# Optimization experiments

Hardware: AMD Instinct MI355X
Metric: run time of the kernel (lower is better)

Reference implementation:

```python
import jax, jax.numpy as jnp
import numpy as np

INPUT_NDIMS = 1024
HIDDEN = 512
LATENT = 50
BATCH = 16384

def setup_inputs() -> dict:
    key = jax.random.key(0)
    ks = jax.random.split(key, 12)
    s = 0.02
    x = jax.random.uniform(ks[0], (BATCH, INPUT_NDIMS), dtype=jnp.float32)
    u = 0.01 + 0.98 * jax.random.uniform(ks[1], (BATCH, LATENT), dtype=jnp.float32)
    W1 = s * jax.random.normal(ks[2], (HIDDEN, INPUT_NDIMS), dtype=jnp.float32)
    b1 = jnp.zeros((HIDDEN,), jnp.float32)
    Wa = s * jax.random.normal(ks[3], (LATENT, HIDDEN), dtype=jnp.float32)
    ba = jnp.zeros((LATENT,), jnp.float32)
    Wb = s * jax.random.normal(ks[4], (LATENT, HIDDEN), dtype=jnp.float32)
    bb = jnp.zeros((LATENT,), jnp.float32)
    W2 = s * jax.random.normal(ks[5], (HIDDEN, LATENT), dtype=jnp.float32)
    b2 = jnp.zeros((HIDDEN,), jnp.float32)
    W3 = s * jax.random.normal(ks[6], (INPUT_NDIMS, HIDDEN), dtype=jnp.float32)
    b3 = jnp.zeros((INPUT_NDIMS,), jnp.float32)
    return dict(x=x, u=u, W1=W1, b1=b1, Wa=Wa, ba=ba, Wb=Wb, bb=bb, W2=W2, b2=b2, W3=W3, b3=b3)

def _stick_segments(v):
    # pi[:, k] = v[:, k] * prod_{j<k} (1 - v[:, j])  -- single O(K) cumprod pass
    cp = jnp.cumprod(1.0 - v, axis=1)                       # inclusive cumprod
    excl = jnp.concatenate([jnp.ones_like(cp[:, :1]), cp[:, :-1]], axis=1)
    return v * excl

def reference(x, u, W1, b1, Wa, ba, Wb, bb, W2, b2, W3, b3):
    # encoder: MLP -> positive Kumaraswamy params alpha (param1), beta (param2)
    h = jax.nn.relu(x @ W1.T + b1)                           # [B, H]
    alpha = jax.nn.softplus(h @ Wa.T + ba) + 1e-4            # [B, K]
    beta = jax.nn.softplus(h @ Wb.T + bb) + 1e-4             # [B, K]
    # Kumaraswamy reparameterized sample: v = (1 - u^(1/beta))^(1/alpha)
    v = jnp.power(1.0 - jnp.power(u, 1.0 / beta), 1.0 / alpha)
    # set_v_K_to_one: force last stick fraction to 1 so segments sum to 1
    v = v.at[:, -1].set(1.0)
    pi = _stick_segments(v)                                  # [B, K], rows sum to 1
    # decoder: MLP with sigmoid output
    h2 = jax.nn.relu(pi @ W2.T + b2)                         # [B, H]
    recon = jax.nn.sigmoid(h2 @ W3.T + b3)                   # [B, D]
    return recon, alpha, beta
```

## Files before the change

kernel.cpp:

```cpp
#include <hip/hip_runtime.h>
#include <hip/hip_bf16.h>

typedef __hip_bfloat16 bf16_t;
typedef __attribute__((ext_vector_type(4))) float f32x4;
typedef __attribute__((ext_vector_type(8))) __bf16 bf16x8;
typedef __attribute__((ext_vector_type(8))) short s16x8;
typedef __attribute__((ext_vector_type(4))) unsigned short u16x4;

#define BATCH 16384
#define NDIM  1024
#define HID   512
#define LAT   50

#define LOG2E 1.44269504088896340736f
#define RLOG2E 0.69314718055994530942f

__device__ __forceinline__ float ex2(float x) { return __builtin_amdgcn_exp2f(x); }
__device__ __forceinline__ float lg2(float x) { return __builtin_amdgcn_logf(x); }
__device__ __forceinline__ float rcp(float x) { return __builtin_amdgcn_rcpf(x); }

__device__ inline unsigned short f2b_u(float f) {
  union { bf16_t b; unsigned short u; } cv; cv.b = __float2bfloat16(f); return cv.u;
}

__device__ __forceinline__ void gload16(const void* src, void* dst_lds) {
  __builtin_amdgcn_global_load_lds(
      reinterpret_cast<const __attribute__((address_space(1))) void*>(
          reinterpret_cast<unsigned long long>(src)),
      reinterpret_cast<__attribute__((address_space(3))) void*>(
          static_cast<unsigned>(reinterpret_cast<unsigned long long>(dst_lds))),
      16, 0, 0);
}

#define WAIT_VMCNT(N)                                          \
  do {                                                         \
    asm volatile("s_waitcnt vmcnt(%0)" ::"i"(N) : "memory");   \
    __builtin_amdgcn_sched_barrier(0);                         \
  } while (0)

__global__ void prep_kernel(const float* __restrict__ x,  const float* __restrict__ W1,
                            const float* __restrict__ W3, const float* __restrict__ Wa,
                            const float* __restrict__ Wb, const float* __restrict__ W2,
                            const float* __restrict__ ba, const float* __restrict__ bb,
                            bf16_t* __restrict__ xb,  bf16_t* __restrict__ w1,
                            bf16_t* __restrict__ w3,  bf16_t* __restrict__ wab,
                            bf16_t* __restrict__ w2p, float* __restrict__ bab)
{
  const int XU   = (BATCH * NDIM) / 4;
  const int W1U  = (HID * NDIM) / 4;
  const int W3U  = (NDIM * HID) / 4;
  const int WABN = 128 * HID;
  const int W2PN = HID * 64;
  const int TOT  = XU + W1U + W3U + WABN + W2PN + 128;
  for (int i = blockIdx.x * blockDim.x + threadIdx.x; i < TOT;
       i += gridDim.x * blockDim.x) {
    int j = i;
    if (j < XU) {
      const f32x4 v = ((const f32x4*)x)[j];
      u16x4 o; o[0]=f2b_u(v[0]); o[1]=f2b_u(v[1]); o[2]=f2b_u(v[2]); o[3]=f2b_u(v[3]);
      ((u16x4*)xb)[j] = o; continue;
    }
    j -= XU;
    if (j < W1U) {
      const f32x4 v = ((const f32x4*)W1)[j];
      u16x4 o; o[0]=f2b_u(v[0]); o[1]=f2b_u(v[1]); o[2]=f2b_u(v[2]); o[3]=f2b_u(v[3]);
      ((u16x4*)w1)[j] = o; continue;
    }
    j -= W1U;
    if (j < W3U) {
      const f32x4 v = ((const f32x4*)W3)[j];
      u16x4 o; o[0]=f2b_u(v[0]); o[1]=f2b_u(v[1]); o[2]=f2b_u(v[2]); o[3]=f2b_u(v[3]);
      ((u16x4*)w3)[j] = o; continue;
    }
    j -= W3U;
    if (j < WABN) {
      const int n = j >> 9, k = j & 511;
      float v = (n < 50) ? Wa[n * 512 + k] : ((n < 100) ? Wb[(n - 50) * 512 + k] : 0.f);
      wab[j] = __float2bfloat16(v); continue;
    }
    j -= WABN;
    if (j < W2PN) {
      const int n = j >> 6, k = j & 63;
      w2p[j] = __float2bfloat16(k < 50 ? W2[n * 50 + k] : 0.f); continue;
    }
    j -= W2PN;
    bab[j] = (j < 50) ? ba[j] : ((j < 100) ? bb[j - 50] : 0.f);
  }
}

template<int EPI, int MT, int NT>
__global__ __launch_bounds__(512, 4)
void gemm_kernel(const bf16_t* __restrict__ A, const bf16_t* __restrict__ B,
                 const float* __restrict__ bias, void* __restrict__ out0,
                 int M, int N, int K)
{
  constexpr int MI  = MT / 32;
  constexpr int NI  = NT / 64;
  constexpr int IA  = MT / 64;
  constexpr int IB  = NT / 64;
  constexpr int L   = IA + IB;
  constexpr int BUF = MT * 128 + NT * 128;
  __shared__ char lds[2 * BUF];

  const int tid  = threadIdx.x;
  const int swzid = ((blockIdx.x & 7) * (gridDim.x >> 3)) + (blockIdx.x >> 3);
  const int nblocks = N / NT;
  const int bn   = swzid % nblocks;
  const int bm   = swzid / nblocks;
  const int wid  = tid >> 6;
  const int lane = tid & 63;
  const int l15  = lane & 15;
  const int l4   = lane >> 4;
  const int wm   = (wid >> 2) * (MT / 2);
  const int wn   = (wid & 3) * (NT / 4);
  const int uw   = __builtin_amdgcn_readfirstlane(wid);

  f32x4 acc[MI][NI] = {};

  auto stage = [&](char* buf, int k0) {
    #pragma unroll
    for (int i = 0; i < IA; ++i) {
      const int c  = (i * 8 + uw) * 64 + lane;
      const int r  = c >> 3;
      const int sp = c & 7;
      const int sl = sp ^ (r & 7);
      gload16(A + (size_t)(bm * MT + r) * K + k0 + sl * 8,
              buf + (i * 8 + uw) * 1024);
    }
    char* lB = buf + MT * 128;
    #pragma unroll
    for (int i = 0; i < IB; ++i) {
      const int c  = (i * 8 + uw) * 64 + lane;
      const int r  = c >> 3;
      const int sp = c & 7;
      const int sl = sp ^ (r & 7);
      gload16(B + (size_t)(bn * NT + r) * K + k0 + sl * 8,
              lB + (i * 8 + uw) * 1024);
    }
  };
  auto compute = [&](const char* buf) {
    const char* lA = buf;
    const char* lB = buf + MT * 128;
    #pragma unroll
    for (int h = 0; h < 2; ++h) {
      bf16x8 af[MI], bfr[NI];
      #pragma unroll
      for (int mi = 0; mi < MI; ++mi) {
        const int row = wm + mi * 16 + l15;
        const int sp  = (h * 4 + l4) ^ (row & 7);
        af[mi] = *(const bf16x8*)(lA + row * 128 + sp * 16);
      }
      #pragma unroll
      for (int ni = 0; ni < NI; ++ni) {
        const int row = wn + ni * 16 + l15;
        const int sp  = (h * 4 + l4) ^ (row & 7);
        bfr[ni] = *(const bf16x8*)(lB + row * 128 + sp * 16);
      }
      #pragma unroll
      for (int mi = 0; mi < MI; ++mi)
        #pragma unroll
        for (int ni = 0; ni < NI; ++ni)
          acc[mi][ni] = __builtin_amdgcn_mfma_f32_16x16x32_bf16(
              af[mi], bfr[ni], acc[mi][ni], 0, 0, 0);
    }
  };

  const int nt = K >> 6;
  stage(lds, 0);
  if (nt > 1) stage(lds + BUF, 64);
  for (int t = 0; t < nt; ++t) {
    if (t + 1 < nt) WAIT_VMCNT(L);
    else            WAIT_VMCNT(0);
    __builtin_amdgcn_s_barrier();
    compute(lds + (t & 1) * BUF);
    __builtin_amdgcn_s_barrier();
    __builtin_amdgcn_sched_barrier(0);
    if (t + 2 < nt) stage(lds + (t & 1) * BUF, (t + 2) << 6);
  }

  #pragma unroll
  for (int ni = 0; ni < NI; ++ni) {
    const int n  = bn * NT + wn + ni * 16 + l15;
    const float bv = bias[n];
    #pragma unroll
    for (int mi = 0; mi < MI; ++mi) {
      #pragma unroll
      for (int r = 0; r < 4; ++r) {
        const int m  = bm * MT + wm + mi * 16 + l4 * 4 + r;
        const float t = acc[mi][ni][r] + bv;
        if (EPI == 0) {
          ((bf16_t*)out0)[(size_t)m * N + n] = __float2bfloat16(fmaxf(t, 0.f));
        } else {
          ((float*)out0)[(size_t)m * N + n] = rcp(1.f + ex2(-t * LOG2E));
        }
      }
    }
  }
}

__global__ __launch_bounds__(512, 2)
void abstick_kernel(const bf16_t* __restrict__ A, const bf16_t* __restrict__ wabg,
                    const float* __restrict__ bab, const bf16_t* __restrict__ w2pg,
                    const float* __restrict__ b2, const float* __restrict__ u,
                    float* __restrict__ out_a, float* __restrict__ out_b,
                    bf16_t* __restrict__ h2)
{
  constexpr int BUF = 64 * 128 + 16384;
  constexpr int PIL = 65536;
  constexpr int SMO = 73728;
  __shared__ char lds[100352];

  const int tid  = threadIdx.x;
  const int swzid = ((blockIdx.x & 7) * (gridDim.x >> 3)) + (blockIdx.x >> 3);
  const int bm   = swzid;
  const int wid  = tid >> 6;
  const int lane = tid & 63;
  const int l15  = lane & 15;
  const int l4   = lane >> 4;
  const int wm   = (wid >> 2) * 32;
  const int wn   = (wid & 3) * 32;
  const int uw   = __builtin_amdgcn_readfirstlane(wid);
  const int K    = HID;

  f32x4 acc[2][2] = {};

  auto stage_AB = [&](char* buf, int k0) {
    {
      const int c  = tid;
      const int r  = c >> 3;
      const int sp = c & 7;
      const int sl = sp ^ (r & 7);
      gload16(A + (size_t)(bm * 64 + r) * K + k0 + sl * 8, buf + uw * 1024);
    }
    char* lB = buf + 8192;
    #pragma unroll
    for (int i = 0; i < 2; ++i) {
      const int c  = (i * 8 + uw) * 64 + lane;
      const int r  = c >> 3;
      const int sp = c & 7;
      const int sl = sp ^ (r & 7);
      gload16(wabg + (size_t)r * K + k0 + sl * 8, lB + (i * 8 + uw) * 1024);
    }
  };
  auto compute1 = [&](const char* buf) {
    const char* lA = buf;
    const char* lB = buf + 8192;
    #pragma unroll
    for (int h = 0; h < 2; ++h) {
      bf16x8 af[2], bfr[2];
      #pragma unroll
      for (int mi = 0; mi < 2; ++mi) {
        const int row = wm + mi * 16 + l15;
        const int sp  = (h * 4 + l4) ^ (row & 7);
        af[mi] = *(const bf16x8*)(lA + row * 128 + sp * 16);
      }
      #pragma unroll
      for (int ni = 0; ni < 2; ++ni) {
        const int row = wn + ni * 16 + l15;
        const int sp  = (h * 4 + l4) ^ (row & 7);
        bfr[ni] = *(const bf16x8*)(lB + row * 128 + sp * 16);
      }
      #pragma unroll
      for (int mi = 0; mi < 2; ++mi)
        #pragma unroll
        for (int ni = 0; ni < 2; ++ni)
          acc[mi][ni] = __builtin_amdgcn_mfma_f32_16x16x32_bf16(
              af[mi], bfr[ni], acc[mi][ni], 0, 0, 0);
    }
  };

  stage_AB(lds, 0);
  stage_AB(lds + BUF, 64);
  for (int t = 0; t < 8; ++t) {
    if (t + 1 < 8) WAIT_VMCNT(3);
    else           WAIT_VMCNT(0);
    __builtin_amdgcn_s_barrier();
    compute1(lds + (t & 1) * BUF);
    __builtin_amdgcn_s_barrier();
    __builtin_amdgcn_sched_barrier(0);
    if (t + 2 < 8) stage_AB(lds + (t & 1) * BUF, (t + 2) << 6);
  }

  #pragma unroll
  for (int i = 0; i < 8; ++i) {
    const int c  = (i * 8 + uw) * 64 + lane;
    const int r  = c >> 3;
    const int sp = c & 7;
    const int sl = sp ^ (r & 7);
    gload16(w2pg + (size_t)r * 64 + sl * 8, lds + (i * 8 + uw) * 1024);
  }

  float* sm = (float*)(lds + SMO);
  #pragma unroll
  for (int ni = 0; ni < 2; ++ni) {
    const int n  = wn + ni * 16 + l15;
    const float bv = bab[n];
    #pragma unroll
    for (int mi = 0; mi < 2; ++mi) {
      #pragma unroll
      for (int r = 0; r < 4; ++r) {
        const int ml = wm + mi * 16 + l4 * 4 + r;
        const int m  = bm * 64 + ml;
        const float t = acc[mi][ni][r] + bv;
        if (n < 100) {
          const float y =
              (t > 20.f ? t : lg2(1.f + ex2(t * LOG2E)) * RLOG2E) + 1e-4f;
          if (n < 50) out_a[(size_t)m * 50 + n] = y;
          else        out_b[(size_t)m * 50 + (n - 50)] = y;
          sm[ml * 104 + n + (n < 50 ? 0 : 2)] = y;
        }
      }
    }
  }
  __syncthreads();

  #pragma unroll 1
  for (int rr = 0; rr < 8; ++rr) {
    const int rl = wid * 8 + rr;
    const size_t m = (size_t)(bm * 64 + rl);
    float v = 1.f, t = 1.f;
    if (lane < 49) {
      const float a  = sm[rl * 104 + lane];
      const float b  = sm[rl * 104 + 52 + lane];
      const float uu = u[m * 50 + lane];
      const float tb = ex2(lg2(uu) * rcp(b));
      v = ex2(lg2(1.f - tb) * rcp(a));
      t = 1.f - v;
    }
    float p = t;
    #pragma unroll
    for (int d = 1; d < 64; d <<= 1) {
      const float o = __shfl_up(p, d, 64);
      if (lane >= d) p *= o;
    }
    float e = __shfl_up(p, 1, 64);
    if (lane == 0) e = 1.f;
    const float piv = (lane < 50) ? v * e : 0.f;
    *(unsigned short*)(lds + PIL + rl * 128 +
                       (((lane >> 3) ^ (rl & 7)) << 4) + ((lane & 7) << 1)) =
        f2b_u(piv);
  }
  __syncthreads();

  const int wn3 = (wid & 3) * 128;
  f32x4 acc3[2][8] = {};
  #pragma unroll
  for (int h = 0; h < 2; ++h) {
    bf16x8 af[2], bfr[8];
    #pragma unroll
    for (int mi = 0; mi < 2; ++mi) {
      const int row = wm + mi * 16 + l15;
      const int sp  = (h * 4 + l4) ^ (row & 7);
      af[mi] = *(const bf16x8*)(lds + PIL + row * 128 + sp * 16);
    }
    #pragma unroll
    for (int ni = 0; ni < 8; ++ni) {
      const int row = wn3 + ni * 16 + l15;
      const int sp  = (h * 4 + l4) ^ (row & 7);
      bfr[ni] = *(const bf16x8*)(lds + row * 128 + sp * 16);
    }
    #pragma unroll
    for (int mi = 0; mi < 2; ++mi)
      #pragma unroll
      for (int ni = 0; ni < 8; ++ni)
        acc3[mi][ni] = __builtin_amdgcn_mfma_f32_16x16x32_bf16(
            af[mi], bfr[ni], acc3[mi][ni], 0, 0, 0);
  }
  #pragma unroll
  for (int ni = 0; ni < 8; ++ni) {
    const int n  = wn3 + ni * 16 + l15;
    const float bv = b2[n];
    #pragma unroll
    for (int mi = 0; mi < 2; ++mi) {
      #pragma unroll
      for (int r = 0; r < 4; ++r) {
        const int m  = bm * 64 + wm + mi * 16 + l4 * 4 + r;
        h2[(size_t)m * HID + n] =
            __float2bfloat16(fmaxf(acc3[mi][ni][r] + bv, 0.f));
      }
    }
  }
}

extern "C" void kernel_launch(void* const* d_in, const int* in_sizes, int n_in,
                              void* d_out, int out_size, void* d_ws, size_t ws_size,
                              hipStream_t stream)
{
  const float* x  = (const float*)d_in[0];
  const float* u  = (const float*)d_in[1];
  const float* W1 = (const float*)d_in[2];
  const float* b1 = (const float*)d_in[3];
  const float* Wa = (const float*)d_in[4];
  const float* ba = (const float*)d_in[5];
  const float* Wb = (const float*)d_in[6];
  const float* bb = (const float*)d_in[7];
  const float* W2 = (const float*)d_in[8];
  const float* b2 = (const float*)d_in[9];
  const float* W3 = (const float*)d_in[10];
  const float* b3 = (const float*)d_in[11];

  float* recon  = (float*)d_out;
  float* oalpha = recon + (size_t)BATCH * NDIM;
  float* obeta  = oalpha + (size_t)BATCH * LAT;

  char* ws = (char*)d_ws;
  bf16_t* xb  = (bf16_t*)(ws);
  bf16_t* h2  = (bf16_t*)(ws);
  bf16_t* h   = (bf16_t*)(ws + 33554432);
  bf16_t* w1  = (bf16_t*)(ws + 50331648);
  bf16_t* w3  = (bf16_t*)(ws + 51380224);
  bf16_t* wab = (bf16_t*)(ws + 52428800);
  bf16_t* w2p = (bf16_t*)(ws + 52559872);
  float*  bab = (float*)(ws + 52625408);

  prep_kernel<<<2048, 256, 0, stream>>>(x, W1, W3, Wa, Wb, W2, ba, bb,
                                        xb, w1, w3, wab, w2p, bab);
  gemm_kernel<0, 64, 256><<<512, 512, 0, stream>>>(
      xb, w1, b1, (void*)h, BATCH, HID, NDIM);
  abstick_kernel<<<256, 512, 0, stream>>>(
      h, wab, bab, w2p, b2, u, oalpha, obeta, h2);
  gemm_kernel<1, 64, 256><<<1024, 512, 0, stream>>>(
      h2, w3, b3, (void*)recon, BATCH, NDIM, HID);
}
```

Measured before the change: 86.57 us.

## Fuse fp32-to-bf16 conversion of x into the first GEMM's A loading

Removes the separate conversion pass over the large input x. The first GEMM now loads fp32 rows into registers, converts them to bf16 and writes them into swizzled LDS itself. The goal is to drop a full write and re-read of the bf16 copy of x. In exchange, the GEMM loses async global-to-LDS loads for A and uses a register-staged double buffer with block barriers, which may expose load latency and increase register pressure.

Result: faster. 80.59 us (-6.9%).

```diff
diff --git a/kernel.cpp b/kernel.cpp
--- a/kernel.cpp
+++ b/kernel.cpp
@@ -38,29 +38,22 @@
     __builtin_amdgcn_sched_barrier(0);                         \
   } while (0)
 
-__global__ void prep_kernel(const float* __restrict__ x,  const float* __restrict__ W1,
-                            const float* __restrict__ W3, const float* __restrict__ Wa,
-                            const float* __restrict__ Wb, const float* __restrict__ W2,
-                            const float* __restrict__ ba, const float* __restrict__ bb,
-                            bf16_t* __restrict__ xb,  bf16_t* __restrict__ w1,
-                            bf16_t* __restrict__ w3,  bf16_t* __restrict__ wab,
-                            bf16_t* __restrict__ w2p, float* __restrict__ bab)
+__global__ void prep_w_kernel(const float* __restrict__ W1, const float* __restrict__ W3,
+                              const float* __restrict__ Wa, const float* __restrict__ Wb,
+                              const float* __restrict__ W2, const float* __restrict__ ba,
+                              const float* __restrict__ bb,
+                              bf16_t* __restrict__ w1, bf16_t* __restrict__ w3,
+                              bf16_t* __restrict__ wab, bf16_t* __restrict__ w2p,
+                              float* __restrict__ bab)
 {
-  const int XU   = (BATCH * NDIM) / 4;
   const int W1U  = (HID * NDIM) / 4;
   const int W3U  = (NDIM * HID) / 4;
   const int WABN = 128 * HID;
   const int W2PN = HID * 64;
-  const int TOT  = XU + W1U + W3U + WABN + W2PN + 128;
+  const int TOT  = W1U + W3U + WABN + W2PN + 128;
   for (int i = blockIdx.x * blockDim.x + threadIdx.x; i < TOT;
        i += gridDim.x * blockDim.x) {
     int j = i;
-    if (j < XU) {
-      const f32x4 v = ((const f32x4*)x)[j];
-      u16x4 o; o[0]=f2b_u(v[0]); o[1]=f2b_u(v[1]); o[2]=f2b_u(v[2]); o[3]=f2b_u(v[3]);
-      ((u16x4*)xb)[j] = o; continue;
-    }
-    j -= XU;
     if (j < W1U) {
       const f32x4 v = ((const f32x4*)W1)[j];
       u16x4 o; o[0]=f2b_u(v[0]); o[1]=f2b_u(v[1]); o[2]=f2b_u(v[2]); o[3]=f2b_u(v[3]);
@@ -88,9 +81,9 @@
   }
 }
 
-template<int EPI, int MT, int NT>
+template<int A_F32, int EPI, int MT, int NT>
 __global__ __launch_bounds__(512, 4)
-void gemm_kernel(const bf16_t* __restrict__ A, const bf16_t* __restrict__ B,
+void gemm_kernel(const void* __restrict__ Av, const bf16_t* __restrict__ B,
                  const float* __restrict__ bias, void* __restrict__ out0,
                  int M, int N, int K)
 {
@@ -116,8 +109,10 @@
   const int uw   = __builtin_amdgcn_readfirstlane(wid);
 
   f32x4 acc[MI][NI] = {};
-
-  auto stage = [&](char* buf, int k0) {
+  f32x4 areg[2 * IA];
+
+  auto stage_A = [&](char* buf, int k0) {
+    const bf16_t* A = (const bf16_t*)Av;
     #pragma unroll
     for (int i = 0; i < IA; ++i) {
       const int c  = (i * 8 + uw) * 64 + lane;
@@ -127,6 +122,34 @@
       gload16(A + (size_t)(bm * MT + r) * K + k0 + sl * 8,
               buf + (i * 8 + uw) * 1024);
     }
+  };
+  auto load_A_f32 = [&](int k0) {
+    const float* A = (const float*)Av;
+    #pragma unroll
+    for (int i = 0; i < IA; ++i) {
+      const int c  = i * 512 + tid;
+      const int r  = c >> 3;
+      const int sl = c & 7;
+      const float* s = A + (size_t)(bm * MT + r) * K + k0 + sl * 8;
+      areg[2 * i]     = *(const f32x4*)s;
+      areg[2 * i + 1] = *(const f32x4*)(s + 4);
+    }
+  };
+  auto write_A_f32 = [&](char* buf) {
+    #pragma unroll
+    for (int i = 0; i < IA; ++i) {
+      const int c  = i * 512 + tid;
+      const int r  = c >> 3;
+      const int sl = c & 7;
+      const int sp = sl ^ (r & 7);
+      union { s16x8 v; unsigned short us[8]; } o;
+      const f32x4 v0 = areg[2 * i], v1 = areg[2 * i + 1];
+      o.us[0]=f2b_u(v0[0]); o.us[1]=f2b_u(v0[1]); o.us[2]=f2b_u(v0[2]); o.us[3]=f2b_u(v0[3]);
+      o.us[4]=f2b_u(v1[0]); o.us[5]=f2b_u(v1[1]); o.us[6]=f2b_u(v1[2]); o.us[7]=f2b_u(v1[3]);
+      *(s16x8*)(buf + r * 128 + sp * 16) = o.v;
+    }
+  };
+  auto stage_B = [&](char* buf, int k0) {
     char* lB = buf + MT * 128;
     #pragma unroll
     for (int i = 0; i < IB; ++i) {
@@ -166,16 +189,34 @@
   };
 
   const int nt = K >> 6;
-  stage(lds, 0);
-  if (nt > 1) stage(lds + BUF, 64);
-  for (int t = 0; t < nt; ++t) {
-    if (t + 1 < nt) WAIT_VMCNT(L);
-    else            WAIT_VMCNT(0);
-    __builtin_amdgcn_s_barrier();
-    compute(lds + (t & 1) * BUF);
-    __builtin_amdgcn_s_barrier();
-    __builtin_amdgcn_sched_barrier(0);
-    if (t + 2 < nt) stage(lds + (t & 1) * BUF, (t + 2) << 6);
+  if constexpr (A_F32) {
+    load_A_f32(0); write_A_f32(lds); stage_B(lds, 0);
+    __syncthreads();
+    int cur = 0;
+    for (int t = 0; t < nt - 1; ++t) {
+      char* nbuf = lds + (cur ^ 1) * BUF;
+      const int k0n = (t + 1) << 6;
+      load_A_f32(k0n);
+      stage_B(nbuf, k0n);
+      compute(lds + cur * BUF);
+      write_A_f32(nbuf);
+      __syncthreads();
+      cur ^= 1;
+    }
+    compute(lds + cur * BUF);
+  } else {
+    stage_A(lds, 0);      stage_B(lds, 0);
+    if (nt > 1) { stage_A(lds + BUF, 64); stage_B(lds + BUF, 64); }
+    for (int t = 0; t < nt; ++t) {
+      if (t + 1 < nt) WAIT_VMCNT(L);
+      else            WAIT_VMCNT(0);
+      __builtin_amdgcn_s_barrier();
+      compute(lds + (t & 1) * BUF);
+      __builtin_amdgcn_s_barrier();
+      __builtin_amdgcn_sched_barrier(0);
+      if (t + 2 < nt) { stage_A(lds + (t & 1) * BUF, (t + 2) << 6);
+                        stage_B(lds + (t & 1) * BUF, (t + 2) << 6); }
+    }
   }
 
   #pragma unroll
@@ -404,21 +445,20 @@
   float* obeta  = oalpha + (size_t)BATCH * LAT;
 
   char* ws = (char*)d_ws;
-  bf16_t* xb  = (bf16_t*)(ws);
   bf16_t* h2  = (bf16_t*)(ws);
-  bf16_t* h   = (bf16_t*)(ws + 33554432);
-  bf16_t* w1  = (bf16_t*)(ws + 50331648);
-  bf16_t* w3  = (bf16_t*)(ws + 51380224);
-  bf16_t* wab = (bf16_t*)(ws + 52428800);
-  bf16_t* w2p = (bf16_t*)(ws + 52559872);
-  float*  bab = (float*)(ws + 52625408);
-
-  prep_kernel<<<2048, 256, 0, stream>>>(x, W1, W3, Wa, Wb, W2, ba, bb,
-                                        xb, w1, w3, wab, w2p, bab);
-  gemm_kernel<0, 64, 256><<<512, 512, 0, stream>>>(
-      xb, w1, b1, (void*)h, BATCH, HID, NDIM);
+  bf16_t* h   = (bf16_t*)(ws + 16777216);
+  bf16_t* w1  = (bf16_t*)(ws + 33554432);
+  bf16_t* w3  = (bf16_t*)(ws + 34603008);
+  bf16_t* wab = (bf16_t*)(ws + 35651584);
+  bf16_t* w2p = (bf16_t*)(ws + 35782656);
+  float*  bab = (float*)(ws + 35848192);
+
+  prep_w_kernel<<<512, 256, 0, stream>>>(W1, W3, Wa, Wb, W2, ba, bb,
+                                         w1, w3, wab, w2p, bab);
+  gemm_kernel<1, 0, 64, 256><<<512, 512, 0, stream>>>(
+      x, w1, b1, (void*)h, BATCH, HID, NDIM);
   abstick_kernel<<<256, 512, 0, stream>>>(
       h, wab, bab, w2p, b2, u, oalpha, obeta, h2);
-  gemm_kernel<1, 64, 256><<<1024, 512, 0, stream>>>(
+  gemm_kernel<0, 1, 64, 256><<<1024, 512, 0, stream>>>(
       h2, w3, b3, (void*)recon, BATCH, NDIM, HID);
 }
```
